# Kernel tuning notes

Hardware: AMD Instinct MI355X
Metric: run time of the kernel (lower is better)

The kernel has to match this reference:

```python
import jax, jax.numpy as jnp
import numpy as np

EPS = 1e-6

def _complex_linear(xr, xi, wr, wi):
    # torch Linear: y = x @ W.T ; complex: (xr+i*xi)(Wr+i*Wi)
    yr = jnp.einsum('bsd,ed->bse', xr, wr) - jnp.einsum('bsd,ed->bse', xi, wi)
    yi = jnp.einsum('bsd,ed->bse', xr, wi) + jnp.einsum('bsd,ed->bse', xi, wr)
    return yr, yi

def setup_inputs() -> dict:
    key = jax.random.key(0)
    ks = jax.random.split(key, 12)
    B, S, D = 32768, 16, 64
    inp = {
        'z_real': jax.random.normal(ks[0], (B, D), jnp.float32),
        'z_imag': jax.random.normal(ks[1], (B, D), jnp.float32),
        'mem':    jax.random.normal(ks[2], (B, S, 2 * D), jnp.float32),
        'ptr':    jax.random.uniform(ks[3], (B, S), jnp.float32),
        'ctrl':   jax.random.normal(ks[4], (B, 3), jnp.float32),
        'wq_r': jax.random.normal(ks[5], (D, D), jnp.float32) / np.sqrt(D),
        'wq_i': jax.random.normal(ks[6], (D, D), jnp.float32) / np.sqrt(D),
        'wk_r': jax.random.normal(ks[7], (D, D), jnp.float32) / np.sqrt(D),
        'wk_i': jax.random.normal(ks[8], (D, D), jnp.float32) / np.sqrt(D),
        'wv_r': jax.random.normal(ks[9], (D, D), jnp.float32) / np.sqrt(D),
        'wv_i': jax.random.normal(ks[10], (D, D), jnp.float32) / np.sqrt(D),
    }
    return inp

def reference(z_real, z_imag, mem, ptr, ctrl, wq_r, wq_i, wk_r, wk_i, wv_r, wv_i):
    D = z_real.shape[-1]
    # soft push/pop/stay gates, normalized
    g = jax.nn.sigmoid(ctrl)  # (B,3)
    push, pop, stay = g[:, 0:1], g[:, 1:2], g[:, 2:3]
    total = push + pop + stay + EPS
    push, pop, stay = push / total, pop / total, stay / total
    # pointer update via rolls
    ptr_up = jnp.roll(ptr, 1, axis=1)
    ptr_down = jnp.roll(ptr, -1, axis=1)
    new_ptr = push * ptr_up + pop * ptr_down + stay * ptr  # (B,S)
    # memory write
    z_flat = jnp.concatenate([z_real, z_imag], axis=-1)  # (B,2D)
    mem_new = mem * (1.0 - push[..., None]) + push[..., None] * z_flat[:, None, :]
    mr, mi = mem_new[..., :D], mem_new[..., D:]  # (B,S,D) complex memory
    # complex attention over stack slots
    qr, qi = _complex_linear(mr, mi, wq_r, wq_i)
    kr, ki = _complex_linear(mr, mi, wk_r, wk_i)
    vr, vi = _complex_linear(mr, mi, wv_r, wv_i)
    q_flat = jnp.concatenate([qr, qi], axis=-1)  # (B,S,2D)
    k_flat = jnp.concatenate([kr, ki], axis=-1)
    scale = D ** (-0.5)
    scores = jnp.einsum('bse,bte->bst', q_flat, k_flat) * scale  # (B,S,S)
    attn = jax.nn.softmax(scores, axis=-1)
    ar = jnp.einsum('bst,btd->bsd', attn, vr)
    ai = jnp.einsum('bst,btd->bsd', attn, vi)
    att_flat = jnp.concatenate([ar, ai], axis=-1)  # (B,S,2D)
    # pointer-weighted read
    read_flat = (att_flat * new_ptr[..., None]).sum(axis=1)  # (B,2D)
    z_read_r, z_read_i = read_flat[:, :D], read_flat[:, D:]
    active_slots = (new_ptr > 0.1).astype(jnp.float32).sum(axis=1).mean()
    return (z_read_r, z_read_i, mem_new, new_ptr, active_slots)
```

## Files before the change

### kernel.cpp

```cpp
#include <hip/hip_runtime.h>


typedef __bf16 bf16x8 __attribute__((ext_vector_type(8)));
typedef float  f32x4  __attribute__((ext_vector_type(4)));
typedef float  f4     __attribute__((ext_vector_type(4)));

#define B_TOT   32768
#define GRID_WG 512
#define NWAVES  4096
#define BPW     8
#define LOG2E   1.4426950408889634f
#define EXSC    0.18033688011112042f

__device__ __forceinline__ unsigned short f2bf(float x) {
  __bf16 h = (__bf16)x;
  return __builtin_bit_cast(unsigned short, h);
}
__device__ __forceinline__ float rcp_f(float x) { return __builtin_amdgcn_rcpf(x); }
__device__ __forceinline__ float ex2_f(float x) { return __builtin_amdgcn_exp2f(x); }
__device__ __forceinline__ float sigm(float x) { return rcp_f(1.0f + ex2_f(-LOG2E * x)); }

__device__ __forceinline__ bf16x8 negbf8(bf16x8 v) {
  uint4 u = __builtin_bit_cast(uint4, v);
  u.x ^= 0x80008000u; u.y ^= 0x80008000u; u.z ^= 0x80008000u; u.w ^= 0x80008000u;
  return __builtin_bit_cast(bf16x8, u);
}

__device__ __forceinline__ float dpp_sum16(float v) {
  int x;
  x = __builtin_amdgcn_update_dpp(0, __builtin_bit_cast(int, v), 0xB1, 0xF, 0xF, false);
  v += __builtin_bit_cast(float, x);
  x = __builtin_amdgcn_update_dpp(0, __builtin_bit_cast(int, v), 0x4E, 0xF, 0xF, false);
  v += __builtin_bit_cast(float, x);
  x = __builtin_amdgcn_update_dpp(0, __builtin_bit_cast(int, v), 0x141, 0xF, 0xF, false);
  v += __builtin_bit_cast(float, x);
  x = __builtin_amdgcn_update_dpp(0, __builtin_bit_cast(int, v), 0x140, 0xF, 0xF, false);
  v += __builtin_bit_cast(float, x);
  return v;
}

__global__ void ems_fin(const unsigned int* __restrict__ c, float* __restrict__ out) {
  if (threadIdx.x == 0) out[0] = (float)(*c) * (1.0f / 32768.0f);
}

__global__ void __launch_bounds__(128)
ems_mt(const float* __restrict__ wqr, const float* __restrict__ wqi,
       const float* __restrict__ wkr, const float* __restrict__ wki,
       unsigned short* __restrict__ mt, unsigned int* __restrict__ cnt)
{
  if (blockIdx.x == 0 && threadIdx.x == 0) *cnt = 0u;
  __shared__ float sK[128];
  const int e2 = (int)blockIdx.x;
  const int e  = (int)threadIdx.x;
  float kv;
  if (e < 64) kv = (e2 < 64) ? wkr[e*64 + e2]      : -wki[e*64 + (e2-64)];
  else        kv = (e2 < 64) ? wki[(e-64)*64 + e2] :  wkr[(e-64)*64 + (e2-64)];
  sK[e] = kv;
  __syncthreads();
  float acc = 0.0f;
  #pragma unroll 8
  for (int Ep = 0; Ep < 64; ++Ep) {
    float q = (e < 64) ? wqr[Ep*64 + e] : -wqi[Ep*64 + (e-64)];
    acc += q * sK[Ep];
  }
  #pragma unroll 8
  for (int Ep = 0; Ep < 64; ++Ep) {
    float q = (e < 64) ? wqi[Ep*64 + e] : wqr[Ep*64 + (e-64)];
    acc += q * sK[64 + Ep];
  }
  mt[e2*128 + e] = f2bf(acc);
}

__global__ void __launch_bounds__(512, 4)
ems_main(const float* __restrict__ z_real, const float* __restrict__ z_imag,
         const float* __restrict__ mem,    const float* __restrict__ ptrv,
         const float* __restrict__ ctrl,
         const float* __restrict__ wvr,    const float* __restrict__ wvi,
         const unsigned short* __restrict__ mt,
         float* __restrict__ out_zr, float* __restrict__ out_zi,
         float* __restrict__ out_mem, float* __restrict__ out_ptr,
         unsigned int* __restrict__ ws_cnt)
{
  __shared__ __align__(16) unsigned short lds[40960];

  const int tid = (int)threadIdx.x;

  for (int idx = tid; idx < 16384; idx += 512) {
    int e2 = idx >> 7, e = idx & 127;
    lds[(e2 << 7) + (((e >> 3) ^ (e2 & 15)) << 3) + (e & 7)] = mt[idx];
  }
  #pragma unroll
  for (int m = 0; m < 2; ++m) {
    const float* wp = m ? wvi : wvr;
    for (int idx = tid; idx < 4096; idx += 512) {
      int e = idx >> 6, d = idx & 63;
      lds[16384 + (m << 12) + (e << 6) + (((d >> 3) ^ (e & 7)) << 3) + (d & 7)] = f2bf(wp[idx]);
    }
  }
  __syncthreads();

  const int lane = tid & 63;
  const int wv   = tid >> 6;
  const int c    = lane & 15;
  const int g    = lane >> 4;
  const int d4   = lane & 31;

  {
    int phase = (wv << 1) | (((int)blockIdx.x >> 8) & 1);
    #pragma unroll 1
    for (int i = 0; i < phase; ++i) __builtin_amdgcn_s_sleep(44);
  }

  unsigned short* SY = &lds[24576 + (wv << 11)];

  const f4* mem4 = (const f4*)mem;
  const f4* zr4  = (const f4*)z_real;
  const f4* zi4  = (const f4*)z_imag;
  f4* omem4 = (f4*)out_mem;

  unsigned int active_acc = 0u;
  const int b0 = (int)blockIdx.x * 8 + wv;

  for (int it = 0; it < BPW; ++it) {
    const int b = b0 + it * NWAVES;

    f4 cm[8];
    #pragma unroll
    for (int k = 0; k < 8; ++k) cm[k] = mem4[b*512 + (k << 6) + lane];
    f4 z4 = (d4 < 16) ? zr4[b*16 + d4] : zi4[b*16 + (d4 - 16)];

    float pu = sigm(ctrl[b*3+0]);
    float po = sigm(ctrl[b*3+1]);
    float st = sigm(ctrl[b*3+2]);
    float rt = rcp_f(pu + po + st + 1e-6f);
    pu *= rt; po *= rt; st *= rt;

    float pm = ptrv[b*16 + ((c+15)&15)];
    float pp = ptrv[b*16 + ((c+ 1)&15)];
    float pc = ptrv[b*16 + c];
    float np = pu*pm + po*pp + st*pc;
    if (g == 0) out_ptr[b*16 + c] = np;
    unsigned long long ball = __ballot(np > 0.1f);
    active_acc += (unsigned int)__popcll(ball & 0xFFFFull);

    float om = 1.0f - pu;
    #pragma unroll
    for (int k = 0; k < 8; ++k) {
      f4 r = cm[k] * om + pu * z4;
      omem4[b*512 + (k << 6) + lane] = r;
      uint2 pk;
      pk.x = (unsigned)f2bf(r[0]) | ((unsigned)f2bf(r[1]) << 16);
      pk.y = (unsigned)f2bf(r[2]) | ((unsigned)f2bf(r[3]) << 16);
      int row = (k << 1) + (lane >> 5);
      *(uint2*)&SY[(row << 7) + (((d4 >> 1) ^ row) << 3) + ((d4 & 1) << 2)] = pk;
    }

    bf16x8 af[4], afn[2];
    #pragma unroll
    for (int t = 0; t < 4; ++t)
      af[t] = *(const bf16x8*)&SY[(c << 7) + ((((t << 2) + g) ^ c) << 3)];
    afn[0] = negbf8(af[2]);
    afn[1] = negbf8(af[3]);

    #pragma unroll
    for (int n2 = 0; n2 < 8; ++n2) {
      int e2 = (n2 << 4) + c;
      f32x4 acc = {0.f,0.f,0.f,0.f};
      #pragma unroll
      for (int T = 0; T < 4; ++T) {
        bf16x8 am = *(const bf16x8*)&lds[(e2 << 7) + ((((T << 2) + g) ^ c) << 3)];
        acc = __builtin_amdgcn_mfma_f32_16x16x32_bf16(am, af[T], acc, 0, 0, 0);
      }
      uint2 pk;
      pk.x = (unsigned)f2bf(acc[0]) | ((unsigned)f2bf(acc[1]) << 16);
      pk.y = (unsigned)f2bf(acc[2]) | ((unsigned)f2bf(acc[3]) << 16);
      *(uint2*)&SY[(c << 7) + ((((n2 << 1) + (g >> 1)) ^ c) << 3) + ((g & 1) << 2)] = pk;
    }

    f32x4 sc = {0.f,0.f,0.f,0.f};
    #pragma unroll
    for (int T = 0; T < 4; ++T) {
      bf16x8 yb = *(const bf16x8*)&SY[(c << 7) + ((((T << 2) + g) ^ c) << 3)];
      sc = __builtin_amdgcn_mfma_f32_16x16x32_bf16(af[T], yb, sc, 0, 0, 0);
    }

    float e0 = ex2_f(sc[0] * EXSC);
    float e1 = ex2_f(sc[1] * EXSC);
    float e2v = ex2_f(sc[2] * EXSC);
    float e3 = ex2_f(sc[3] * EXSC);
    float r = (e0 + e1) + (e2v + e3);
    r += __shfl_xor(r, 16, 64);
    r += __shfl_xor(r, 32, 64);
    float u = np * rcp_f(r);
    float w4[4];
    w4[0] = dpp_sum16(u * e0);
    w4[1] = dpp_sum16(u * e1);
    w4[2] = dpp_sum16(u * e2v);
    w4[3] = dpp_sum16(u * e3);

    #pragma unroll
    for (int n = 0; n < 4; ++n) {
      int eb = 16384 + (((n << 4) + c) << 6);
      int e7 = c & 7;
      f32x4 ar = {0.f,0.f,0.f,0.f}, ai = {0.f,0.f,0.f,0.f};
      #pragma unroll
      for (int t = 0; t < 2; ++t) {
        int ch = (((t << 2) + g) ^ e7) << 3;
        bf16x8 fr = *(const bf16x8*)&lds[eb + ch];
        bf16x8 fi = *(const bf16x8*)&lds[eb + 4096 + ch];
        ar = __builtin_amdgcn_mfma_f32_16x16x32_bf16(af[t],   fr, ar, 0,0,0);
        ai = __builtin_amdgcn_mfma_f32_16x16x32_bf16(af[t],   fi, ai, 0,0,0);
        ar = __builtin_amdgcn_mfma_f32_16x16x32_bf16(afn[t],  fi, ar, 0,0,0);
        ai = __builtin_amdgcn_mfma_f32_16x16x32_bf16(af[t+2], fr, ai, 0,0,0);
      }
      float prr = ar[0]*w4[0] + ar[1]*w4[1] + ar[2]*w4[2] + ar[3]*w4[3];
      float pri = ai[0]*w4[0] + ai[1]*w4[1] + ai[2]*w4[2] + ai[3]*w4[3];
      prr += __shfl_xor(prr, 16, 64);
      prr += __shfl_xor(prr, 32, 64);
      pri += __shfl_xor(pri, 16, 64);
      pri += __shfl_xor(pri, 32, 64);
      if (g == 0) out_zr[b*64 + (n << 4) + c] = prr;
      if (g == 1) out_zi[b*64 + (n << 4) + c] = pri;
    }
  }

  __syncthreads();
  unsigned int* cnt_lds = (unsigned int*)&lds[24576];
  if (tid == 0) *cnt_lds = 0u;
  __syncthreads();
  if (lane == 0) atomicAdd(cnt_lds, active_acc);
  __syncthreads();
  if (tid == 0) atomicAdd(ws_cnt, *cnt_lds);
}

extern "C" void kernel_launch(void* const* d_in, const int* in_sizes, int n_in,
                              void* d_out, int out_size, void* d_ws, size_t ws_size,
                              hipStream_t stream) {
  const float* z_real = (const float*)d_in[0];
  const float* z_imag = (const float*)d_in[1];
  const float* memp   = (const float*)d_in[2];
  const float* ptrv   = (const float*)d_in[3];
  const float* ctrl   = (const float*)d_in[4];
  const float* wq_r   = (const float*)d_in[5];
  const float* wq_i   = (const float*)d_in[6];
  const float* wk_r   = (const float*)d_in[7];
  const float* wk_i   = (const float*)d_in[8];
  const float* wv_r   = (const float*)d_in[9];
  const float* wv_i   = (const float*)d_in[10];

  float* out     = (float*)d_out;
  float* out_zr  = out;
  float* out_zi  = out + 2097152;
  float* out_mem = out + 4194304;
  float* out_ptr = out + 71303168;
  float* out_sc  = out + 71827456;

  unsigned int*   cnt = (unsigned int*)d_ws;
  unsigned short* mtp = (unsigned short*)((char*)d_ws + 1024);

  ems_mt<<<128, 128, 0, stream>>>(wq_r, wq_i, wk_r, wk_i, mtp, cnt);
  ems_main<<<GRID_WG, 512, 0, stream>>>(z_real, z_imag, memp, ptrv, ctrl,
                                        wv_r, wv_i, mtp,
                                        out_zr, out_zi, out_mem, out_ptr, cnt);
  ems_fin<<<1, 64, 0, stream>>>(cnt, out_sc);
}
```

Before: 146.3 us.

## Process two batches per wave iteration to share weight LDS loads

```diff
diff --git a/kernel.cpp b/kernel.cpp
--- a/kernel.cpp
+++ b/kernel.cpp
@@ -8,7 +8,7 @@
 #define B_TOT   32768
 #define GRID_WG 512
 #define NWAVES  4096
-#define BPW     8
+#define PAIRS   4
 #define LOG2E   1.4426950408889634f
 #define EXSC    0.18033688011112042f
 
@@ -108,10 +108,11 @@
   {
     int phase = (wv << 1) | (((int)blockIdx.x >> 8) & 1);
     #pragma unroll 1
-    for (int i = 0; i < phase; ++i) __builtin_amdgcn_s_sleep(44);
-  }
-
-  unsigned short* SY = &lds[24576 + (wv << 11)];
+    for (int i = 0; i < phase; ++i) __builtin_amdgcn_s_sleep(88);
+  }
+
+  unsigned short* SY  = &lds[24576 + (wv << 11)];
+  unsigned short* SYB = SY + 1024;
 
   const f4* mem4 = (const f4*)mem;
   const f4* zr4  = (const f4*)z_real;
@@ -121,9 +122,7 @@
   unsigned int active_acc = 0u;
   const int b0 = (int)blockIdx.x * 8 + wv;
 
-  for (int it = 0; it < BPW; ++it) {
-    const int b = b0 + it * NWAVES;
-
+  auto stageBatch = [&](int b, bf16x8* af, bf16x8* afn, float& np_out) {
     f4 cm[8];
     #pragma unroll
     for (int k = 0; k < 8; ++k) cm[k] = mem4[b*512 + (k << 6) + lane];
@@ -134,7 +133,6 @@
     float st = sigm(ctrl[b*3+2]);
     float rt = rcp_f(pu + po + st + 1e-6f);
     pu *= rt; po *= rt; st *= rt;
-
     float pm = ptrv[b*16 + ((c+15)&15)];
     float pp = ptrv[b*16 + ((c+ 1)&15)];
     float pc = ptrv[b*16 + c];
@@ -142,6 +140,7 @@
     if (g == 0) out_ptr[b*16 + c] = np;
     unsigned long long ball = __ballot(np > 0.1f);
     active_acc += (unsigned int)__popcll(ball & 0xFFFFull);
+    np_out = np;
 
     float om = 1.0f - pu;
     #pragma unroll
@@ -154,73 +153,109 @@
       int row = (k << 1) + (lane >> 5);
       *(uint2*)&SY[(row << 7) + (((d4 >> 1) ^ row) << 3) + ((d4 & 1) << 2)] = pk;
     }
-
-    bf16x8 af[4], afn[2];
     #pragma unroll
     for (int t = 0; t < 4; ++t)
       af[t] = *(const bf16x8*)&SY[(c << 7) + ((((t << 2) + g) ^ c) << 3)];
     afn[0] = negbf8(af[2]);
     afn[1] = negbf8(af[3]);
-
-    #pragma unroll
-    for (int n2 = 0; n2 < 8; ++n2) {
-      int e2 = (n2 << 4) + c;
-      f32x4 acc = {0.f,0.f,0.f,0.f};
+  };
+
+  #pragma unroll 1
+  for (int it = 0; it < PAIRS; ++it) {
+    const int bA = b0 + (2*it)     * NWAVES;
+    const int bB = b0 + (2*it + 1) * NWAVES;
+
+    bf16x8 afA[4], afnA[2], afB[4], afnB[2];
+    float npA, npB;
+    stageBatch(bA, afA, afnA, npA);
+    stageBatch(bB, afB, afnB, npB);
+
+    f32x4 scA = {0.f,0.f,0.f,0.f}, scB = {0.f,0.f,0.f,0.f};
+    #pragma unroll
+    for (int h = 0; h < 2; ++h) {
       #pragma unroll
-      for (int T = 0; T < 4; ++T) {
-        bf16x8 am = *(const bf16x8*)&lds[(e2 << 7) + ((((T << 2) + g) ^ c) << 3)];
-        acc = __builtin_amdgcn_mfma_f32_16x16x32_bf16(am, af[T], acc, 0, 0, 0);
-      }
-      uint2 pk;
-      pk.x = (unsigned)f2bf(acc[0]) | ((unsigned)f2bf(acc[1]) << 16);
-      pk.y = (unsigned)f2bf(acc[2]) | ((unsigned)f2bf(acc[3]) << 16);
-      *(uint2*)&SY[(c << 7) + ((((n2 << 1) + (g >> 1)) ^ c) << 3) + ((g & 1) << 2)] = pk;
-    }
-
-    f32x4 sc = {0.f,0.f,0.f,0.f};
-    #pragma unroll
-    for (int T = 0; T < 4; ++T) {
-      bf16x8 yb = *(const bf16x8*)&SY[(c << 7) + ((((T << 2) + g) ^ c) << 3)];
-      sc = __builtin_amdgcn_mfma_f32_16x16x32_bf16(af[T], yb, sc, 0, 0, 0);
-    }
-
-    float e0 = ex2_f(sc[0] * EXSC);
-    float e1 = ex2_f(sc[1] * EXSC);
-    float e2v = ex2_f(sc[2] * EXSC);
-    float e3 = ex2_f(sc[3] * EXSC);
-    float r = (e0 + e1) + (e2v + e3);
-    r += __shfl_xor(r, 16, 64);
-    r += __shfl_xor(r, 32, 64);
-    float u = np * rcp_f(r);
-    float w4[4];
-    w4[0] = dpp_sum16(u * e0);
-    w4[1] = dpp_sum16(u * e1);
-    w4[2] = dpp_sum16(u * e2v);
-    w4[3] = dpp_sum16(u * e3);
+      for (int n2 = 0; n2 < 4; ++n2) {
+        int e2 = (h << 6) + (n2 << 4) + c;
+        f32x4 aA = {0.f,0.f,0.f,0.f}, aB = {0.f,0.f,0.f,0.f};
+        #pragma unroll
+        for (int T = 0; T < 4; ++T) {
+          bf16x8 am = *(const bf16x8*)&lds[(e2 << 7) + ((((T << 2) + g) ^ c) << 3)];
+          aA = __builtin_amdgcn_mfma_f32_16x16x32_bf16(am, afA[T], aA, 0, 0, 0);
+          aB = __builtin_amdgcn_mfma_f32_16x16x32_bf16(am, afB[T], aB, 0, 0, 0);
+        }
+        int off = (c << 6) + ((((n2 << 1) + (g >> 1)) ^ (c & 7)) << 3) + ((g & 1) << 2);
+        uint2 pkA, pkB;
+        pkA.x = (unsigned)f2bf(aA[0]) | ((unsigned)f2bf(aA[1]) << 16);
+        pkA.y = (unsigned)f2bf(aA[2]) | ((unsigned)f2bf(aA[3]) << 16);
+        pkB.x = (unsigned)f2bf(aB[0]) | ((unsigned)f2bf(aB[1]) << 16);
+        pkB.y = (unsigned)f2bf(aB[2]) | ((unsigned)f2bf(aB[3]) << 16);
+        *(uint2*)&SY[off]  = pkA;
+        *(uint2*)&SYB[off] = pkB;
+      }
+      #pragma unroll
+      for (int Tp = 0; Tp < 2; ++Tp) {
+        int off = (c << 6) + ((((Tp << 2) + g) ^ (c & 7)) << 3);
+        bf16x8 yA = *(const bf16x8*)&SY[off];
+        bf16x8 yB = *(const bf16x8*)&SYB[off];
+        scA = __builtin_amdgcn_mfma_f32_16x16x32_bf16(afA[(h << 1) + Tp], yA, scA, 0, 0, 0);
+        scB = __builtin_amdgcn_mfma_f32_16x16x32_bf16(afB[(h << 1) + Tp], yB, scB, 0, 0, 0);
+      }
+    }
+
+    float w4A[4], w4B[4];
+    {
+      float e0 = ex2_f(scA[0]*EXSC), e1 = ex2_f(scA[1]*EXSC);
+      float e2v = ex2_f(scA[2]*EXSC), e3 = ex2_f(scA[3]*EXSC);
+      float f0 = ex2_f(scB[0]*EXSC), f1 = ex2_f(scB[1]*EXSC);
+      float f2v = ex2_f(scB[2]*EXSC), f3 = ex2_f(scB[3]*EXSC);
+      float rA = (e0 + e1) + (e2v + e3);
+      float rB = (f0 + f1) + (f2v + f3);
+      rA += __shfl_xor(rA, 16, 64);  rB += __shfl_xor(rB, 16, 64);
+      rA += __shfl_xor(rA, 32, 64);  rB += __shfl_xor(rB, 32, 64);
+      float uA = npA * rcp_f(rA);
+      float uB = npB * rcp_f(rB);
+      w4A[0] = dpp_sum16(uA * e0);  w4B[0] = dpp_sum16(uB * f0);
+      w4A[1] = dpp_sum16(uA * e1);  w4B[1] = dpp_sum16(uB * f1);
+      w4A[2] = dpp_sum16(uA * e2v); w4B[2] = dpp_sum16(uB * f2v);
+      w4A[3] = dpp_sum16(uA * e3);  w4B[3] = dpp_sum16(uB * f3);
+    }
 
     #pragma unroll
     for (int n = 0; n < 4; ++n) {
       int eb = 16384 + (((n << 4) + c) << 6);
       int e7 = c & 7;
-      f32x4 ar = {0.f,0.f,0.f,0.f}, ai = {0.f,0.f,0.f,0.f};
+      f32x4 arA = {0.f,0.f,0.f,0.f}, aiA = {0.f,0.f,0.f,0.f};
+      f32x4 arB = {0.f,0.f,0.f,0.f}, aiB = {0.f,0.f,0.f,0.f};
       #pragma unroll
       for (int t = 0; t < 2; ++t) {
         int ch = (((t << 2) + g) ^ e7) << 3;
         bf16x8 fr = *(const bf16x8*)&lds[eb + ch];
         bf16x8 fi = *(const bf16x8*)&lds[eb + 4096 + ch];
-        ar = __builtin_amdgcn_mfma_f32_16x16x32_bf16(af[t],   fr, ar, 0,0,0);
-        ai = __builtin_amdgcn_mfma_f32_16x16x32_bf16(af[t],   fi, ai, 0,0,0);
-        ar = __builtin_amdgcn_mfma_f32_16x16x32_bf16(afn[t],  fi, ar, 0,0,0);
-        ai = __builtin_amdgcn_mfma_f32_16x16x32_bf16(af[t+2], fr, ai, 0,0,0);
-      }
-      float prr = ar[0]*w4[0] + ar[1]*w4[1] + ar[2]*w4[2] + ar[3]*w4[3];
-      float pri = ai[0]*w4[0] + ai[1]*w4[1] + ai[2]*w4[2] + ai[3]*w4[3];
-      prr += __shfl_xor(prr, 16, 64);
-      prr += __shfl_xor(prr, 32, 64);
-      pri += __shfl_xor(pri, 16, 64);
-      pri += __shfl_xor(pri, 32, 64);
-      if (g == 0) out_zr[b*64 + (n << 4) + c] = prr;
-      if (g == 1) out_zi[b*64 + (n << 4) + c] = pri;
+        arA = __builtin_amdgcn_mfma_f32_16x16x32_bf16(afA[t],   fr, arA, 0,0,0);
+        arB = __builtin_amdgcn_mfma_f32_16x16x32_bf16(afB[t],   fr, arB, 0,0,0);
+        aiA = __builtin_amdgcn_mfma_f32_16x16x32_bf16(afA[t],   fi, aiA, 0,0,0);
+        aiB = __builtin_amdgcn_mfma_f32_16x16x32_bf16(afB[t],   fi, aiB, 0,0,0);
+        arA = __builtin_amdgcn_mfma_f32_16x16x32_bf16(afnA[t],  fi, arA, 0,0,0);
+        arB = __builtin_amdgcn_mfma_f32_16x16x32_bf16(afnB[t],  fi, arB, 0,0,0);
+        aiA = __builtin_amdgcn_mfma_f32_16x16x32_bf16(afA[t+2], fr, aiA, 0,0,0);
+        aiB = __builtin_amdgcn_mfma_f32_16x16x32_bf16(afB[t+2], fr, aiB, 0,0,0);
+      }
+      float prrA = arA[0]*w4A[0] + arA[1]*w4A[1] + arA[2]*w4A[2] + arA[3]*w4A[3];
+      float priA = aiA[0]*w4A[0] + aiA[1]*w4A[1] + aiA[2]*w4A[2] + aiA[3]*w4A[3];
+      float prrB = arB[0]*w4B[0] + arB[1]*w4B[1] + arB[2]*w4B[2] + arB[3]*w4B[3];
+      float priB = aiB[0]*w4B[0] + aiB[1]*w4B[1] + aiB[2]*w4B[2] + aiB[3]*w4B[3];
+      prrA += __shfl_xor(prrA, 16, 64);  prrB += __shfl_xor(prrB, 16, 64);
+      prrA += __shfl_xor(prrA, 32, 64);  prrB += __shfl_xor(prrB, 32, 64);
+      priA += __shfl_xor(priA, 16, 64);  priB += __shfl_xor(priB, 16, 64);
+      priA += __shfl_xor(priA, 32, 64);  priB += __shfl_xor(priB, 32, 64);
+      if (g == 0) {
+        out_zr[bA*64 + (n << 4) + c] = prrA;
+        out_zr[bB*64 + (n << 4) + c] = prrB;
+      }
+      if (g == 1) {
+        out_zi[bA*64 + (n << 4) + c] = priA;
+        out_zi[bB*64 + (n << 4) + c] = priB;
+      }
     }
   }
 
```

Measured after the change: 152.1 us. 3.9% more time.
